# Kernel tuning notes

Measured on AMD Instinct MI355X. Metric: run time of the kernel, lower is better.

## Reference

```python
import jax, jax.numpy as jnp
import numpy as np

N = 2048      # layer_size
R = 4         # displacement rank
B = 4096      # batch
STD = 0.01    # init_stddev


def toeplitz_mult(G, H, x):
    """out[b] = sum_i Krylov(Z_1, g_i) @ Krylov(Z_{-1}, h_i)^T @ x[b]   (cycle=True, f=(1,-1)).

    Krylov(Z_1, g) is the circulant matrix C(g) with first column g:
        C(g)[i, j] = g[(i-j) mod n]
    Krylov(Z_{-1}, h) is the skew-circulant S(h):
        S(h)[i, j] = h[(i-j) mod n] * (-1 if i < j else 1)
    Using the factorization S(h) = D^{-1} C(D h) D with D = diag(eta^k), eta = exp(i*pi/n):
        S(h)^T x = D C((D h)') D^{-1} x,   where c'[k] = c[(-k) mod n]
    and circulant products are done via FFT: C(c) u = ifft(fft(c) * fft(u)).
    """
    r, n = G.shape
    eta = jnp.exp(1j * jnp.pi * jnp.arange(n) / n).astype(jnp.complex64)  # (n,)
    # ---- transpose Krylov multiply with f = -1:  U_i = S(h_i)^T x,  shape (r, b, n) ----
    Hm = H.astype(jnp.complex64) * eta                      # D h_i, (r, n)
    Hm_rev = jnp.roll(Hm[:, ::-1], 1, axis=-1)              # c'[k] = c[(-k) mod n]
    xm = x.astype(jnp.complex64) / eta                      # D^{-1} x, (b, n)
    U = jnp.fft.ifft(jnp.fft.fft(Hm_rev)[:, None, :] * jnp.fft.fft(xm)[None, :, :], axis=-1)
    U = (U * eta).real                                      # S(h_i)^T x is real, (r, b, n)
    # ---- Krylov multiply with f = 1:  Y_i = C(g_i) U_i ----
    Gf = jnp.fft.fft(G.astype(jnp.complex64))[:, None, :]   # (r, 1, n)
    Y = jnp.fft.ifft(Gf * jnp.fft.fft(U.astype(jnp.complex64), axis=-1), axis=-1).real
    return Y.sum(0)                                         # (b, n)


def setup_inputs() -> dict:
    key = jax.random.key(0)
    k1, k2, k3 = jax.random.split(key, 3)
    x = jax.random.normal(k1, (B, N), jnp.float32)
    G = jax.random.normal(k2, (R, N), jnp.float32) * STD
    H = jax.random.normal(k3, (R, N), jnp.float32) * STD
    return {"x": x, "G": G, "H": H}


def reference(x, G, H):
    return toeplitz_mult(G, H, x)
```

## Files before the change

kernel.cpp:

```cpp
#include <hip/hip_runtime.h>
#include <cstdint>
#include <cstddef>

constexpr int kN = 2048;
constexpr int kB = 4096;
constexpr int kR = 4;

typedef __attribute__((ext_vector_type(4))) float f32x4;
typedef __attribute__((ext_vector_type(8))) short short8;
typedef __attribute__((ext_vector_type(8))) unsigned short ushort8;

__device__ __forceinline__ unsigned short f2bf(float f) {
  unsigned u = __float_as_uint(f);
  u += 0x7FFFu + ((u >> 16) & 1u);
  return (unsigned short)(u >> 16);
}

__device__ __forceinline__ void gload_lds16(const void* g, void* l) {
  __builtin_amdgcn_global_load_lds(
      (const __attribute__((address_space(1))) void*)g,
      (__attribute__((address_space(3))) void*)l, 16, 0, 0);
}

__global__ void cast_x_kernel(const float* __restrict__ x,
                              unsigned short* __restrict__ xb) {
  const int t = blockIdx.x * blockDim.x + threadIdx.x;
  const float4* xv = (const float4*)x;
  float4 a = xv[t * 2];
  float4 b = xv[t * 2 + 1];
  ushort8 o;
  o[0] = f2bf(a.x); o[1] = f2bf(a.y); o[2] = f2bf(a.z); o[3] = f2bf(a.w);
  o[4] = f2bf(b.x); o[5] = f2bf(b.y); o[6] = f2bf(b.z); o[7] = f2bf(b.w);
  *(ushort8*)(xb + (size_t)t * 8) = o;
}

__global__ void build_D_kernel(const float* __restrict__ G,
                               const float* __restrict__ H,
                               unsigned short* __restrict__ Dp) {
  const int d = blockIdx.x;
  const int tid = threadIdx.x;
  const int lane = tid & 63, wave = tid >> 6;
  const int v0 = tid * 8;

  float loc[8];
  float run = 0.f;
#pragma unroll
  for (int jj = 0; jj < 8; ++jj) {
    const int v = v0 + jj;
    float q = 0.f;
#pragma unroll
    for (int t = 0; t < kR; ++t)
      q += G[t * kN + ((v + d) & (kN - 1))] * H[t * kN + v];
    run += q;
    loc[jj] = run;
  }

  float incl = run;
#pragma unroll
  for (int off = 1; off < 64; off <<= 1) {
    float tv = __shfl_up(incl, off, 64);
    if (lane >= off) incl += tv;
  }
  __shared__ float wsum[4];
  if (lane == 63) wsum[wave] = incl;
  __syncthreads();
  float woff = 0.f, total = 0.f;
#pragma unroll
  for (int w = 0; w < 4; ++w) {
    const float s = wsum[w];
    total += s;
    if (w < wave) woff += s;
  }
  const float exc = woff + incl - run;

  ushort8 o;
#pragma unroll
  for (int jj = 0; jj < 8; ++jj)
    o[jj] = f2bf(2.f * (exc + loc[jj]) - total);
  *(ushort8*)(Dp + (size_t)d * kN + v0) = o;
}

__global__ void build_M_kernel(const unsigned short* __restrict__ Dp,
                               unsigned short* __restrict__ Mb) {
  __shared__ unsigned short lds[128][64];
  const int tid = threadIdx.x;
  const int i0 = blockIdx.y * 64, j0 = blockIdx.x * 64;
  const int delta0 = (i0 - j0 - 63) & (kN - 1);
#pragma unroll
  for (int it = 0; it < 32; ++it) {
    const int lin = it * 256 + tid;
    const int dd = lin >> 6, jj = lin & 63;
    lds[dd][jj] = Dp[(size_t)((delta0 + dd) & (kN - 1)) * kN + j0 + jj];
  }
  __syncthreads();
#pragma unroll
  for (int it = 0; it < 16; ++it) {
    const int lin = it * 256 + tid;
    const int ii = lin >> 6, jj = lin & 63;
    Mb[(size_t)(i0 + ii) * kN + j0 + jj] = lds[ii - jj + 63][jj];
  }
}

__global__ __launch_bounds__(256) void gemm_kernel(
    const unsigned short* __restrict__ A,
    const unsigned short* __restrict__ Bt,
    float* __restrict__ C) {
  __shared__ unsigned short As[128][32];
  __shared__ unsigned short Bs[128][32];

  const int tid = threadIdx.x;
  const int lane = tid & 63, wave = tid >> 6;
  const int wr = wave >> 1, wc = wave & 1;
  const int r16 = lane & 15, kg = lane >> 4;
  const int row0 = blockIdx.y * 128;
  const int col0 = blockIdx.x * 128;

  f32x4 acc[4][4] = {};

  const int srow = tid >> 2;
  const int scol = (tid & 3) * 8;

  for (int k0 = 0; k0 < kN; k0 += 32) {
    __syncthreads();
#pragma unroll
    for (int s = 0; s < 2; ++s) {
      gload_lds16(A + (size_t)(row0 + s * 64 + srow) * kN + k0 + scol,
                  (char*)As + s * 4096 + wave * 1024);
      gload_lds16(Bt + (size_t)(col0 + s * 64 + srow) * kN + k0 + scol,
                  (char*)Bs + s * 4096 + wave * 1024);
    }
    __syncthreads();

    short8 af[4], bf[4];
#pragma unroll
    for (int mt = 0; mt < 4; ++mt)
      af[mt] = *(const short8*)&As[wr * 64 + mt * 16 + r16][kg * 8];
#pragma unroll
    for (int nt = 0; nt < 4; ++nt)
      bf[nt] = *(const short8*)&Bs[wc * 64 + nt * 16 + r16][kg * 8];
#pragma unroll
    for (int mt = 0; mt < 4; ++mt)
#pragma unroll
      for (int nt = 0; nt < 4; ++nt)
        acc[mt][nt] = __builtin_amdgcn_mfma_f32_16x16x32_bf16(
            af[mt], bf[nt], acc[mt][nt], 0, 0, 0);
  }

#pragma unroll
  for (int mt = 0; mt < 4; ++mt)
#pragma unroll
    for (int nt = 0; nt < 4; ++nt) {
      const int r = row0 + wr * 64 + mt * 16 + kg * 4;
      const int c = col0 + wc * 64 + nt * 16 + r16;
#pragma unroll
      for (int j = 0; j < 4; ++j)
        C[(size_t)(r + j) * kN + c] = acc[mt][nt][j];
    }
}

extern "C" void kernel_launch(void* const* d_in, const int* in_sizes, int n_in,
                              void* d_out, int out_size, void* d_ws, size_t ws_size,
                              hipStream_t stream) {
  const float* x = (const float*)d_in[0];
  const float* G = (const float*)d_in[1];
  const float* H = (const float*)d_in[2];
  float* out = (float*)d_out;

  char* ws = (char*)d_ws;
  unsigned short* Mb = (unsigned short*)ws;
  unsigned short* xb = (unsigned short*)(ws + (8u << 20));
  unsigned short* Dp = (unsigned short*)(ws + (24u << 20));

  cast_x_kernel<<<dim3((kB * kN) / (256 * 8)), dim3(256), 0, stream>>>(x, xb);
  build_D_kernel<<<dim3(kN), dim3(256), 0, stream>>>(G, H, Dp);
  build_M_kernel<<<dim3(kN / 64, kN / 64), dim3(256), 0, stream>>>(Dp, Mb);
  gemm_kernel<<<dim3(kN / 128, kB / 128), dim3(256), 0, stream>>>(xb, Mb, out);
}
```

Measured before the change: 179.7 us.

## Merge prep kernels, shrink GEMM tile to 128x64, swizzle block order

Fuses the x-to-bf16 cast and the D-diagonal build into one launch, with block index selecting the role. Halves the GEMM N tile to 64 columns, so each wave computes a 64x32 sub-tile and there are twice as many blocks. Remaps blocks with a swizzle of stride 8 for L2 locality. The aim is to cut launch overhead and improve occupancy and wave balance on the many CUs, at the cost of lower arithmetic intensity per block and more reloading of A.

```diff
diff --git a/kernel.cpp b/kernel.cpp
--- a/kernel.cpp
+++ b/kernel.cpp
@@ -22,23 +22,27 @@
       (__attribute__((address_space(3))) void*)l, 16, 0, 0);
 }
 
-__global__ void cast_x_kernel(const float* __restrict__ x,
-                              unsigned short* __restrict__ xb) {
-  const int t = blockIdx.x * blockDim.x + threadIdx.x;
-  const float4* xv = (const float4*)x;
-  float4 a = xv[t * 2];
-  float4 b = xv[t * 2 + 1];
-  ushort8 o;
-  o[0] = f2bf(a.x); o[1] = f2bf(a.y); o[2] = f2bf(a.z); o[3] = f2bf(a.w);
-  o[4] = f2bf(b.x); o[5] = f2bf(b.y); o[6] = f2bf(b.z); o[7] = f2bf(b.w);
-  *(ushort8*)(xb + (size_t)t * 8) = o;
-}
+__global__ void prep_kernel(const float* __restrict__ x,
+                            const float* __restrict__ G,
+                            const float* __restrict__ H,
+                            unsigned short* __restrict__ xb,
+                            unsigned short* __restrict__ Dp) {
+  __shared__ float wsum[4];
+  const int tid = threadIdx.x;
 
-__global__ void build_D_kernel(const float* __restrict__ G,
-                               const float* __restrict__ H,
-                               unsigned short* __restrict__ Dp) {
-  const int d = blockIdx.x;
-  const int tid = threadIdx.x;
+  if (blockIdx.x < (kB * kN) / (256 * 8)) {
+    const int t = blockIdx.x * 256 + tid;
+    const float4* xv = (const float4*)x;
+    float4 a = xv[t * 2];
+    float4 b = xv[t * 2 + 1];
+    ushort8 o;
+    o[0] = f2bf(a.x); o[1] = f2bf(a.y); o[2] = f2bf(a.z); o[3] = f2bf(a.w);
+    o[4] = f2bf(b.x); o[5] = f2bf(b.y); o[6] = f2bf(b.z); o[7] = f2bf(b.w);
+    *(ushort8*)(xb + (size_t)t * 8) = o;
+    return;
+  }
+
+  const int d = blockIdx.x - (kB * kN) / (256 * 8);
   const int lane = tid & 63, wave = tid >> 6;
   const int v0 = tid * 8;
 
@@ -61,7 +65,6 @@
     float tv = __shfl_up(incl, off, 64);
     if (lane >= off) incl += tv;
   }
-  __shared__ float wsum[4];
   if (lane == 63) wsum[wave] = incl;
   __syncthreads();
   float woff = 0.f, total = 0.f;
@@ -106,16 +109,20 @@
     const unsigned short* __restrict__ Bt,
     float* __restrict__ C) {
   __shared__ unsigned short As[128][32];
-  __shared__ unsigned short Bs[128][32];
+  __shared__ unsigned short Bs[64][32];
 
   const int tid = threadIdx.x;
   const int lane = tid & 63, wave = tid >> 6;
   const int wr = wave >> 1, wc = wave & 1;
   const int r16 = lane & 15, kg = lane >> 4;
-  const int row0 = blockIdx.y * 128;
-  const int col0 = blockIdx.x * 128;
 
-  f32x4 acc[4][4] = {};
+  const int flat = blockIdx.y * gridDim.x + blockIdx.x;
+  const int swz = (flat & 7) * 128 + (flat >> 3);
+  const int by = swz >> 5, bx = swz & 31;
+  const int row0 = by * 128;
+  const int col0 = bx * 64;
+
+  f32x4 acc[4][2] = {};
 
   const int srow = tid >> 2;
   const int scol = (tid & 3) * 8;
@@ -123,25 +130,24 @@
   for (int k0 = 0; k0 < kN; k0 += 32) {
     __syncthreads();
 #pragma unroll
-    for (int s = 0; s < 2; ++s) {
+    for (int s = 0; s < 2; ++s)
       gload_lds16(A + (size_t)(row0 + s * 64 + srow) * kN + k0 + scol,
                   (char*)As + s * 4096 + wave * 1024);
-      gload_lds16(Bt + (size_t)(col0 + s * 64 + srow) * kN + k0 + scol,
-                  (char*)Bs + s * 4096 + wave * 1024);
-    }
+    gload_lds16(Bt + (size_t)(col0 + srow) * kN + k0 + scol,
+                (char*)Bs + wave * 1024);
     __syncthreads();
 
-    short8 af[4], bf[4];
+    short8 af[4], bf[2];
 #pragma unroll
     for (int mt = 0; mt < 4; ++mt)
       af[mt] = *(const short8*)&As[wr * 64 + mt * 16 + r16][kg * 8];
 #pragma unroll
-    for (int nt = 0; nt < 4; ++nt)
-      bf[nt] = *(const short8*)&Bs[wc * 64 + nt * 16 + r16][kg * 8];
+    for (int nt = 0; nt < 2; ++nt)
+      bf[nt] = *(const short8*)&Bs[wc * 32 + nt * 16 + r16][kg * 8];
 #pragma unroll
     for (int mt = 0; mt < 4; ++mt)
 #pragma unroll
-      for (int nt = 0; nt < 4; ++nt)
+      for (int nt = 0; nt < 2; ++nt)
         acc[mt][nt] = __builtin_amdgcn_mfma_f32_16x16x32_bf16(
             af[mt], bf[nt], acc[mt][nt], 0, 0, 0);
   }
@@ -149,9 +155,9 @@
 #pragma unroll
   for (int mt = 0; mt < 4; ++mt)
 #pragma unroll
-    for (int nt = 0; nt < 4; ++nt) {
+    for (int nt = 0; nt < 2; ++nt) {
       const int r = row0 + wr * 64 + mt * 16 + kg * 4;
-      const int c = col0 + wc * 64 + nt * 16 + r16;
+      const int c = col0 + wc * 32 + nt * 16 + r16;
 #pragma unroll
       for (int j = 0; j < 4; ++j)
         C[(size_t)(r + j) * kN + c] = acc[mt][nt][j];
@@ -171,8 +177,8 @@
   unsigned short* xb = (unsigned short*)(ws + (8u << 20));
   unsigned short* Dp = (unsigned short*)(ws + (24u << 20));
 
-  cast_x_kernel<<<dim3((kB * kN) / (256 * 8)), dim3(256), 0, stream>>>(x, xb);
-  build_D_kernel<<<dim3(kN), dim3(256), 0, stream>>>(G, H, Dp);
+  const int cast_blocks = (kB * kN) / (256 * 8);
+  prep_kernel<<<dim3(cast_blocks + kN), dim3(256), 0, stream>>>(x, G, H, xb, Dp);
   build_M_kernel<<<dim3(kN / 64, kN / 64), dim3(256), 0, stream>>>(Dp, Mb);
-  gemm_kernel<<<dim3(kN / 128, kB / 128), dim3(256), 0, stream>>>(xb, Mb, out);
+  gemm_kernel<<<dim3(kN / 64, kB / 128), dim3(256), 0, stream>>>(xb, Mb, out);
 }
```

Result: faster. 175.5 us (-2.4%).
